# Optimization experiments

Measured on AMD Instinct MI355X. Metric: run time of the kernel, lower is better.

The kernel has to match this reference:

```python
import jax, jax.numpy as jnp
import numpy as np

D_MODEL = 1024
NUM_HEADS = 16
LN_EPS = 1e-5


def setup_inputs() -> dict:
    key = jax.random.key(0)
    ks = jax.random.split(key, 8)
    d = D_MODEL
    x = jax.random.normal(ks[0], (8, 1024, d), dtype=jnp.float32)
    # nn.MultiheadAttention parameters (combined in_proj, out_proj)
    in_proj_w = jax.random.normal(ks[1], (3 * d, d), dtype=jnp.float32) / np.sqrt(d)
    in_proj_b = jnp.zeros((3 * d,), dtype=jnp.float32)
    out_proj_w = jax.random.normal(ks[2], (d, d), dtype=jnp.float32) / np.sqrt(d)
    out_proj_b = jnp.zeros((d,), dtype=jnp.float32)
    ln_w = jnp.ones((d,), dtype=jnp.float32)
    ln_b = jnp.zeros((d,), dtype=jnp.float32)
    time_decay = jnp.asarray(0.1, dtype=jnp.float32)
    return {"x": x, "time_decay": time_decay, "in_proj_w": in_proj_w,
            "in_proj_b": in_proj_b, "out_proj_w": out_proj_w,
            "out_proj_b": out_proj_b, "ln_w": ln_w, "ln_b": ln_b}


def reference(x, time_decay, in_proj_w, in_proj_b, out_proj_w, out_proj_b, ln_w, ln_b):
    B, S, d = x.shape
    H = NUM_HEADS
    hd = d // H
    # vectorized time-decay bias: -|time_decay| * |i - j|  (replaces nested loop)
    idx = jnp.arange(S, dtype=jnp.float32)
    attn_bias = -jnp.abs(time_decay) * jnp.abs(idx[:, None] - idx[None, :])  # [S,S]
    # combined QKV projection
    qkv = x @ in_proj_w.T + in_proj_b  # [B,S,3d]
    q, k, v = jnp.split(qkv, 3, axis=-1)
    q = q.reshape(B, S, H, hd)
    k = k.reshape(B, S, H, hd)
    v = v.reshape(B, S, H, hd)
    scale = 1.0 / np.sqrt(hd)
    scores = jnp.einsum('bqhd,bkhd->bhqk', q, k) * scale + attn_bias  # [B,H,S,S]
    weights = jax.nn.softmax(scores, axis=-1)
    attn = jnp.einsum('bhqk,bkhd->bqhd', weights, v).reshape(B, S, d)
    attn_out = attn @ out_proj_w.T + out_proj_b
    # need_weights=True with default average_attn_weights=True -> mean over heads
    attn_weights = jnp.mean(weights, axis=1)  # [B,S,S]
    # residual + LayerNorm
    y = x + attn_out
    mu = jnp.mean(y, axis=-1, keepdims=True)
    var = jnp.mean(jnp.square(y - mu), axis=-1, keepdims=True)
    out = (y - mu) / jnp.sqrt(var + LN_EPS) * ln_w + ln_b
    return (out, attn_weights)
```

## Files before the change

### kernel.cpp

```cpp
#include <hip/hip_runtime.h>
#include <cstddef>

#define BATCH   8
#define SEQ     1024
#define DMODEL  1024
#define NHEAD   16
#define HDIM    64
#define D3      3072
#define NROWS   (BATCH * SEQ)
#define LN_EPS  1e-5f

typedef __attribute__((ext_vector_type(4))) float f32x4;
typedef __attribute__((ext_vector_type(8))) short bf16x8;

__device__ __forceinline__ float b2f(unsigned short u) {
    union { unsigned int i; float f; } v; v.i = ((unsigned int)u) << 16; return v.f;
}
__device__ __forceinline__ unsigned short f2bu(float f) {
    union { float f; unsigned int i; } v; v.f = f;
    unsigned int r = v.i + 0x7fffu + ((v.i >> 16) & 1u);
    return (unsigned short)(r >> 16);
}
__device__ __forceinline__ void gl16(const void* g, void* l) {
    __builtin_amdgcn_global_load_lds(
        (const __attribute__((address_space(1))) unsigned int*)g,
        (__attribute__((address_space(3))) unsigned int*)l, 16, 0, 0);
}

#define NG_X  1048576
#define NG_WQ 393216
#define NG_WO 131072
__global__ __launch_bounds__(256)
void cvt_bf16(const float* __restrict__ x, const float* __restrict__ wq,
              const float* __restrict__ wo,
              unsigned short* __restrict__ xb, unsigned short* __restrict__ wqb,
              unsigned short* __restrict__ wob) {
    const int gidx = blockIdx.x * 256 + threadIdx.x;
    const float* src; unsigned short* dst; size_t off;
    if (gidx < NG_X)              { src = x;  dst = xb;  off = (size_t)gidx * 8; }
    else if (gidx < NG_X + NG_WQ) { src = wq; dst = wqb; off = (size_t)(gidx - NG_X) * 8; }
    else                          { src = wo; dst = wob; off = (size_t)(gidx - NG_X - NG_WQ) * 8; }
    float4 v0 = *(const float4*)(src + off);
    float4 v1 = *(const float4*)(src + off + 4);
    uint4 pv;
    pv.x = f2bu(v0.x) | ((unsigned int)f2bu(v0.y) << 16);
    pv.y = f2bu(v0.z) | ((unsigned int)f2bu(v0.w) << 16);
    pv.z = f2bu(v1.x) | ((unsigned int)f2bu(v1.y) << 16);
    pv.w = f2bu(v1.z) | ((unsigned int)f2bu(v1.w) << 16);
    *(uint4*)(dst + off) = pv;
}

__global__ __launch_bounds__(256)
void qkv_mfma(const unsigned short* __restrict__ xb,
              const unsigned short* __restrict__ wb,
              const float* __restrict__ bias,
              unsigned short* __restrict__ qh,
              unsigned short* __restrict__ kh,
              unsigned short* __restrict__ vt) {
    __shared__ unsigned short smem[8192];
    unsigned short* As = smem;
    unsigned short* Bs = smem + 4096;

    const int t = threadIdx.x;
    const int w = t >> 6, lane = t & 63;
    const int wm = w >> 1, wn = w & 1;
    const int g = lane >> 4, c = lane & 15;
    const int m0 = blockIdx.y * 128, n0 = blockIdx.x * 128;

    const int srow = t >> 2;
    const int scol = (t & 3) * 8;
    const unsigned short* ga = xb + (size_t)(m0 + srow) * 1024 + scol;
    const unsigned short* gb = wb + (size_t)(n0 + srow) * 1024 + scol;

    f32x4 acc[4][4];
#pragma unroll
    for (int i = 0; i < 4; ++i)
#pragma unroll
        for (int j = 0; j < 4; ++j) acc[i][j] = (f32x4){0.f, 0.f, 0.f, 0.f};

    for (int k0 = 0; k0 < 1024; k0 += 32) {
        gl16(ga + k0,             As + t * 8);
        gl16(ga + 64 * 1024 + k0, As + 2048 + t * 8);
        gl16(gb + k0,             Bs + t * 8);
        gl16(gb + 64 * 1024 + k0, Bs + 2048 + t * 8);
        __syncthreads();
        bf16x8 af[4], bf[4];
#pragma unroll
        for (int i = 0; i < 4; ++i)
            af[i] = *(const bf16x8*)(As + (wm * 64 + i * 16 + c) * 32 + g * 8);
#pragma unroll
        for (int j = 0; j < 4; ++j)
            bf[j] = *(const bf16x8*)(Bs + (wn * 64 + j * 16 + c) * 32 + g * 8);
#pragma unroll
        for (int i = 0; i < 4; ++i)
#pragma unroll
            for (int j = 0; j < 4; ++j)
                acc[i][j] = __builtin_amdgcn_mfma_f32_16x16x32_bf16(af[i], bf[j], acc[i][j], 0, 0, 0);
        __syncthreads();
    }

    float bsv[4];
#pragma unroll
    for (int j = 0; j < 4; ++j) bsv[j] = bias[n0 + wn * 64 + j * 16 + c];

    unsigned short* eslice = smem + w * 2048;
    const int b_ = m0 >> 10;

    if (n0 < 2048) {
        const int ncl   = n0 + wn * 64;
        unsigned short* dst = (ncl < 1024)
            ? qh + ((size_t)(b_ * 16 + (ncl >> 6)) * 1024) * 64
            : kh + ((size_t)(b_ * 16 + ((ncl - 1024) >> 6)) * 1024) * 64;
#pragma unroll
        for (int half = 0; half < 2; ++half) {
#pragma unroll
            for (int ii = 0; ii < 2; ++ii) {
                const int i = half * 2 + ii;
#pragma unroll
                for (int j = 0; j < 4; ++j)
#pragma unroll
                    for (int r = 0; r < 4; ++r)
                        eslice[(ii * 16 + g * 4 + r) * 64 + j * 16 + c] = f2bu(acc[i][j][r] + bsv[j]);
            }
#pragma unroll
            for (int u = 0; u < 4; ++u) {
                const int mloc = u * 8 + (lane >> 3);
                const int ncol = (lane & 7) * 8;
                bf16x8 row = *(const bf16x8*)(eslice + mloc * 64 + ncol);
                const int tok = (m0 & 1023) + wm * 64 + half * 32 + mloc;
                *(bf16x8*)(dst + (size_t)tok * 64 + ncol) = row;
            }
        }
    } else {
        const int key0  = (m0 & 1023) + wm * 64;
        const int hbase = (n0 + wn * 64 - 2048) >> 6;
#pragma unroll
        for (int half = 0; half < 2; ++half) {
#pragma unroll
            for (int jj = 0; jj < 2; ++jj) {
                const int j = half * 2 + jj;
                const int nloc = jj * 16 + c;
#pragma unroll
                for (int i = 0; i < 4; ++i)
#pragma unroll
                    for (int r = 0; r < 4; ++r) {
                        const int mloc  = i * 16 + g * 4 + r;
                        const int mphys = mloc ^ ((nloc & 7) << 3);
                        eslice[nloc * 64 + mphys] = f2bu(acc[i][j][r] + bsv[j]);
                    }
            }
#pragma unroll
            for (int u = 0; u < 4; ++u) {
                const int nloc  = u * 8 + (lane >> 3);
                const int mb    = lane & 7;
                const int mphys = (mb ^ (nloc & 7)) * 8;
                bf16x8 row = *(const bf16x8*)(eslice + nloc * 64 + mphys);
                const int d = half * 32 + nloc;
                *(bf16x8*)(vt + ((size_t)((b_ * 16 + hbase) * 64 + d)) * 1024 + key0 + mb * 8) = row;
            }
        }
    }
}

__global__ __launch_bounds__(512, 2)
void attn_mfma(const unsigned short* __restrict__ qh,
               const unsigned short* __restrict__ kh,
               const unsigned short* __restrict__ vt,
               const float* __restrict__ tdp,
               unsigned short* __restrict__ attnb,
               float* __restrict__ wout) {
    const int flat = blockIdx.x;
    const int b    = flat & 7;
    const int rest = flat >> 3;
    const int hg   = rest >> 4;
    const int qt   = rest & 15;

    const int t  = threadIdx.x;
    const int w  = t >> 6;
    const int lane = t & 63;
    const int g  = lane >> 4;
    const int c  = lane & 15;

    const int q0 = qt * 64;
    const float td2 = -fabsf(tdp[0]) * 1.44269504f;
    const float sc2 = 0.125f * 1.44269504f;

    __shared__ unsigned short P_s[64][1032];
    __shared__ float rs_s[8][64];
    __shared__ float rs_tot[64];
    __shared__ float Ored[4][4][16][17];

    float wsum[4][8][4];
#pragma unroll
    for (int i = 0; i < 4; ++i)
#pragma unroll
        for (int tt = 0; tt < 8; ++tt)
#pragma unroll
            for (int r = 0; r < 4; ++r) wsum[i][tt][r] = 0.f;

    const int key_base = w * 128;
    const float kf0 = (float)(key_base + c);

    for (int hi = 0; hi < 8; ++hi) {
        const int h = hg * 8 + hi;
        const unsigned short* qslab = qh + (size_t)(b * 16 + h) * 1024 * 64;
        const unsigned short* kslab = kh + (size_t)(b * 16 + h) * 1024 * 64;

        bf16x8 qa[4][2];
#pragma unroll
        for (int i = 0; i < 4; ++i) {
            const unsigned short* qp = qslab + (size_t)(q0 + i * 16 + c) * 64 + g * 8;
            qa[i][0] = *(const bf16x8*)(qp);
            qa[i][1] = *(const bf16x8*)(qp + 32);
        }

        float rsum[4][4];
#pragma unroll
        for (int i = 0; i < 4; ++i)
#pragma unroll
            for (int r = 0; r < 4; ++r) rsum[i][r] = 0.f;

#pragma unroll 2
        for (int tt = 0; tt < 8; ++tt) {
            const int key = key_base + tt * 16 + c;
            const unsigned short* kp = kslab + (size_t)key * 64 + g * 8;
            bf16x8 kb0 = *(const bf16x8*)(kp);
            bf16x8 kb1 = *(const bf16x8*)(kp + 32);
            f32x4 z[4];
#pragma unroll
            for (int i = 0; i < 4; ++i) z[i] = (f32x4){0.f, 0.f, 0.f, 0.f};
#pragma unroll
            for (int i = 0; i < 4; ++i)
                z[i] = __builtin_amdgcn_mfma_f32_16x16x32_bf16(qa[i][0], kb0, z[i], 0, 0, 0);
#pragma unroll
            for (int i = 0; i < 4; ++i)
                z[i] = __builtin_amdgcn_mfma_f32_16x16x32_bf16(qa[i][1], kb1, z[i], 0, 0, 0);
            const float kf = kf0 + (float)(tt * 16);
#pragma unroll
            for (int i = 0; i < 4; ++i) {
#pragma unroll
                for (int r = 0; r < 4; ++r) {
                    const float qf = (float)(q0 + i * 16 + g * 4 + r);
                    const float e = __builtin_amdgcn_exp2f(z[i][r] * sc2 + td2 * fabsf(kf - qf));
                    rsum[i][r] += e;
                    P_s[i * 16 + g * 4 + r][key_base + tt * 16 + c] = f2bu(e);
                }
            }
        }
#pragma unroll
        for (int i = 0; i < 4; ++i)
#pragma unroll
            for (int r = 0; r < 4; ++r) {
                rsum[i][r] += __shfl_xor(rsum[i][r], 1, 64);
                rsum[i][r] += __shfl_xor(rsum[i][r], 2, 64);
                rsum[i][r] += __shfl_xor(rsum[i][r], 4, 64);
                rsum[i][r] += __shfl_xor(rsum[i][r], 8, 64);
            }
        if (c == 0) {
#pragma unroll
            for (int i = 0; i < 4; ++i)
#pragma unroll
                for (int r = 0; r < 4; ++r) rs_s[w][i * 16 + g * 4 + r] = rsum[i][r];
        }
        __syncthreads();

        if (t < 64) {
            float s = 0.f;
#pragma unroll
            for (int j = 0; j < 8; ++j) s += rs_s[j][t];
            rs_tot[t] = 1.0f / s;
        }
        __syncthreads();

        float invl[4][4];
#pragma unroll
        for (int i = 0; i < 4; ++i)
#pragma unroll
            for (int r = 0; r < 4; ++r)
                invl[i][r] = rs_tot[i * 16 + g * 4 + r];

        const int dsl = (w & 3) * 16;
        const int ks0 = (w >> 2) * 16;
        f32x4 accO[4];
#pragma unroll
        for (int i = 0; i < 4; ++i) accO[i] = (f32x4){0.f, 0.f, 0.f, 0.f};
        const unsigned short* vhp = vt + (size_t)((b * 16 + h) * 64 + dsl + c) * 1024;
#pragma unroll 4
        for (int ks = ks0; ks < ks0 + 16; ++ks) {
            bf16x8 vb = *(const bf16x8*)(vhp + ks * 32 + g * 8);
#pragma unroll
            for (int i = 0; i < 4; ++i) {
                bf16x8 pa = *(const bf16x8*)(&P_s[i * 16 + c][ks * 32 + g * 8]);
                accO[i] = __builtin_amdgcn_mfma_f32_16x16x32_bf16(pa, vb, accO[i], 0, 0, 0);
            }
        }
        if (w >= 4) {
#pragma unroll
            for (int i = 0; i < 4; ++i)
#pragma unroll
                for (int r = 0; r < 4; ++r)
                    Ored[w - 4][i][g * 4 + r][c] = accO[i][r];
        }
        __syncthreads();
        if (w < 4) {
            unsigned short* op = attnb + (size_t)(b * 1024 + q0) * 1024 + h * 64 + dsl + c;
#pragma unroll
            for (int i = 0; i < 4; ++i)
#pragma unroll
                for (int r = 0; r < 4; ++r) {
                    const float o = accO[i][r] + Ored[w][i][g * 4 + r][c];
                    op[(size_t)(i * 16 + g * 4 + r) * 1024] = f2bu(o * invl[i][r]);
                }
        }

#pragma unroll
        for (int i = 0; i < 4; ++i)
#pragma unroll
            for (int tt = 0; tt < 8; ++tt)
#pragma unroll
                for (int r = 0; r < 4; ++r)
                    wsum[i][tt][r] += b2f(P_s[i * 16 + g * 4 + r][key_base + tt * 16 + c]) * invl[i][r];
        __syncthreads();
    }

#pragma unroll
    for (int i = 0; i < 4; ++i)
#pragma unroll
        for (int tt = 0; tt < 8; ++tt)
#pragma unroll
            for (int r = 0; r < 4; ++r) {
                atomicAdd(&wout[(size_t)(b * 1024 + q0 + i * 16 + g * 4 + r) * 1024
                                 + key_base + tt * 16 + c],
                          wsum[i][tt][r] * (1.0f / NHEAD));
            }
}

__global__ __launch_bounds__(256)
void outproj_mfma(const unsigned short* __restrict__ ab,
                  const unsigned short* __restrict__ wob,
                  const float* __restrict__ bias,
                  const float* __restrict__ X,
                  float* __restrict__ Y) {
    __shared__ unsigned short smem[8192];
    unsigned short* As = smem;
    unsigned short* Bs = smem + 4096;

    const int t = threadIdx.x;
    const int w = t >> 6, lane = t & 63;
    const int wm = w >> 1, wn = w & 1;
    const int g = lane >> 4, c = lane & 15;
    const int m0 = blockIdx.y * 128, n0 = blockIdx.x * 128;

    const int srow = t >> 2;
    const int scol = (t & 3) * 8;
    const unsigned short* ga = ab  + (size_t)(m0 + srow) * 1024 + scol;
    const unsigned short* gb = wob + (size_t)(n0 + srow) * 1024 + scol;

    f32x4 acc[4][4];
#pragma unroll
    for (int i = 0; i < 4; ++i)
#pragma unroll
        for (int j = 0; j < 4; ++j) acc[i][j] = (f32x4){0.f, 0.f, 0.f, 0.f};

    for (int k0 = 0; k0 < 1024; k0 += 32) {
        gl16(ga + k0,             As + t * 8);
        gl16(ga + 64 * 1024 + k0, As + 2048 + t * 8);
        gl16(gb + k0,             Bs + t * 8);
        gl16(gb + 64 * 1024 + k0, Bs + 2048 + t * 8);
        __syncthreads();
        bf16x8 af[4], bf[4];
#pragma unroll
    for (int i = 0; i < 4; ++i)
            af[i] = *(const bf16x8*)(As + (wm * 64 + i * 16 + c) * 32 + g * 8);
#pragma unroll
        for (int j = 0; j < 4; ++j)
            bf[j] = *(const bf16x8*)(Bs + (wn * 64 + j * 16 + c) * 32 + g * 8);
#pragma unroll
        for (int i = 0; i < 4; ++i)
#pragma unroll
            for (int j = 0; j < 4; ++j)
                acc[i][j] = __builtin_amdgcn_mfma_f32_16x16x32_bf16(af[i], bf[j], acc[i][j], 0, 0, 0);
        __syncthreads();
    }

    float bsv[4];
#pragma unroll
    for (int j = 0; j < 4; ++j) bsv[j] = bias[n0 + wn * 64 + j * 16 + c];

#pragma unroll
    for (int i = 0; i < 4; ++i) {
#pragma unroll
        for (int r = 0; r < 4; ++r) {
            const int m = m0 + wm * 64 + i * 16 + g * 4 + r;
#pragma unroll
            for (int j = 0; j < 4; ++j) {
                const int n = n0 + wn * 64 + j * 16 + c;
                Y[(size_t)m * 1024 + n] = acc[i][j][r] + bsv[j] + X[(size_t)m * 1024 + n];
            }
        }
    }
}

__global__ __launch_bounds__(256)
void ln_kernel(const float* __restrict__ Y, const float* __restrict__ lnw,
               const float* __restrict__ lnb, float* __restrict__ out) {
    const int row = blockIdx.x, t = threadIdx.x;
    __shared__ float rs[256], rq[256];
    const float4 v = ((const float4*)(Y + (size_t)row * DMODEL))[t];
    rs[t] = v.x + v.y + v.z + v.w;
    rq[t] = v.x * v.x + v.y * v.y + v.z * v.z + v.w * v.w;
    __syncthreads();
    for (int off = 128; off > 0; off >>= 1) {
        if (t < off) { rs[t] += rs[t + off]; rq[t] += rq[t + off]; }
        __syncthreads();
    }
    const float mu   = rs[0] * (1.0f / DMODEL);
    const float var  = rq[0] * (1.0f / DMODEL) - mu * mu;
    const float rstd = rsqrtf(var + LN_EPS);
    const float4 w  = ((const float4*)lnw)[t];
    const float4 bb = ((const float4*)lnb)[t];
    float4 o;
    o.x = (v.x - mu) * rstd * w.x + bb.x;
    o.y = (v.y - mu) * rstd * w.y + bb.y;
    o.z = (v.z - mu) * rstd * w.z + bb.z;
    o.w = (v.w - mu) * rstd * w.w + bb.w;
    ((float4*)(out + (size_t)row * DMODEL))[t] = o;
}

extern "C" void kernel_launch(void* const* d_in, const int* in_sizes, int n_in,
                              void* d_out, int out_size, void* d_ws, size_t ws_size,
                              hipStream_t stream) {
    (void)in_sizes; (void)n_in; (void)out_size; (void)ws_size;
    const float* x    = (const float*)d_in[0];
    const float* td   = (const float*)d_in[1];
    const float* wqkv = (const float*)d_in[2];
    const float* bqkv = (const float*)d_in[3];
    const float* wo   = (const float*)d_in[4];
    const float* bo   = (const float*)d_in[5];
    const float* lnw  = (const float*)d_in[6];
    const float* lnb  = (const float*)d_in[7];

    float* out_ln = (float*)d_out;
    float* out_w  = (float*)d_out + (size_t)NROWS * SEQ;

    unsigned short* qh = (unsigned short*)d_ws;
    unsigned short* kh = qh + (size_t)128 * 1024 * 64;
    unsigned short* vt = kh + (size_t)128 * 1024 * 64;
    float*          y  = (float*)d_ws;

    unsigned short* attnb = (unsigned short*)d_out;
    unsigned short* wob   = (unsigned short*)d_out + (size_t)NROWS * DMODEL;
    unsigned short* xb    = (unsigned short*)out_w;
    unsigned short* wqkvb = xb + (size_t)NROWS * DMODEL;

    cvt_bf16    <<<(NG_X + NG_WQ + NG_WO) / 256, 256, 0, stream>>>(x, wqkv, wo, xb, wqkvb, wob);
    qkv_mfma    <<<dim3(D3 / 128, NROWS / 128), 256, 0, stream>>>(xb, wqkvb, bqkv, qh, kh, vt);
    (void)hipMemsetAsync(out_w, 0, (size_t)BATCH * SEQ * SEQ * sizeof(float), stream);
    attn_mfma   <<<dim3(256), 512, 0, stream>>>(qh, kh, vt, td, attnb, out_w);
    outproj_mfma<<<dim3(DMODEL / 128, NROWS / 128), 256, 0, stream>>>(attnb, wob, bo, x, y);
    ln_kernel   <<<NROWS,                       256, 0, stream>>>(y, lnw, lnb, out_ln);
}
```

Measured before the change: 420.9 us.

## Split PV work by query tiles and vectorize head-averaged weight accumulation

The P·V stage now assigns each wave two full query-row tiles over all 32 key steps instead of splitting keys across wave halves. This removes the Ored shared-memory cross-wave reduction and one block barrier per head. The head-averaged weight accumulation is remapped so each thread owns a row and 128 contiguous keys, reading P with 16-byte vector loads in a rotated chunk order to spread LDS bank use. Atomics become row-contiguous per thread. In exchange, the per-thread accumulator shape changes and each wave runs a longer serial MFMA chain.

```diff
diff --git a/kernel.cpp b/kernel.cpp
--- a/kernel.cpp
+++ b/kernel.cpp
@@ -188,15 +188,15 @@
     __shared__ unsigned short P_s[64][1032];
     __shared__ float rs_s[8][64];
     __shared__ float rs_tot[64];
-    __shared__ float Ored[4][4][16][17];
-
-    float wsum[4][8][4];
-#pragma unroll
-    for (int i = 0; i < 4; ++i)
-#pragma unroll
-        for (int tt = 0; tt < 8; ++tt)
-#pragma unroll
-            for (int r = 0; r < 4; ++r) wsum[i][tt][r] = 0.f;
+
+    const int wrow = t >> 3;
+    const int wk0  = (t & 7) * 128;
+    const int crot = t & 7;
+    float wsum[16][8];
+#pragma unroll
+    for (int ch = 0; ch < 16; ++ch)
+#pragma unroll
+        for (int e = 0; e < 8; ++e) wsum[ch][e] = 0.f;
 
     const int key_base = w * 128;
     const float kf0 = (float)(key_base + c);
@@ -272,67 +272,56 @@
         }
         __syncthreads();
 
-        float invl[4][4];
-#pragma unroll
-        for (int i = 0; i < 4; ++i)
-#pragma unroll
-            for (int r = 0; r < 4; ++r)
-                invl[i][r] = rs_tot[i * 16 + g * 4 + r];
-
+        const int tb  = (w >> 2) * 2;
         const int dsl = (w & 3) * 16;
-        const int ks0 = (w >> 2) * 16;
-        f32x4 accO[4];
-#pragma unroll
-        for (int i = 0; i < 4; ++i) accO[i] = (f32x4){0.f, 0.f, 0.f, 0.f};
+        f32x4 accO[2];
+        accO[0] = (f32x4){0.f, 0.f, 0.f, 0.f};
+        accO[1] = (f32x4){0.f, 0.f, 0.f, 0.f};
         const unsigned short* vhp = vt + (size_t)((b * 16 + h) * 64 + dsl + c) * 1024;
 #pragma unroll 4
-        for (int ks = ks0; ks < ks0 + 16; ++ks) {
+        for (int ks = 0; ks < 32; ++ks) {
             bf16x8 vb = *(const bf16x8*)(vhp + ks * 32 + g * 8);
 #pragma unroll
-            for (int i = 0; i < 4; ++i) {
-                bf16x8 pa = *(const bf16x8*)(&P_s[i * 16 + c][ks * 32 + g * 8]);
+            for (int i = 0; i < 2; ++i) {
+                bf16x8 pa = *(const bf16x8*)(&P_s[(tb + i) * 16 + c][ks * 32 + g * 8]);
                 accO[i] = __builtin_amdgcn_mfma_f32_16x16x32_bf16(pa, vb, accO[i], 0, 0, 0);
             }
         }
-        if (w >= 4) {
-#pragma unroll
-            for (int i = 0; i < 4; ++i)
-#pragma unroll
-                for (int r = 0; r < 4; ++r)
-                    Ored[w - 4][i][g * 4 + r][c] = accO[i][r];
-        }
-        __syncthreads();
-        if (w < 4) {
+        {
             unsigned short* op = attnb + (size_t)(b * 1024 + q0) * 1024 + h * 64 + dsl + c;
 #pragma unroll
-            for (int i = 0; i < 4; ++i)
+            for (int i = 0; i < 2; ++i)
 #pragma unroll
                 for (int r = 0; r < 4; ++r) {
-                    const float o = accO[i][r] + Ored[w][i][g * 4 + r][c];
-                    op[(size_t)(i * 16 + g * 4 + r) * 1024] = f2bu(o * invl[i][r]);
+                    const int row = (tb + i) * 16 + g * 4 + r;
+                    op[(size_t)row * 1024] = f2bu(accO[i][r] * rs_tot[row]);
                 }
         }
 
-#pragma unroll
-        for (int i = 0; i < 4; ++i)
-#pragma unroll
-            for (int tt = 0; tt < 8; ++tt)
-#pragma unroll
-                for (int r = 0; r < 4; ++r)
-                    wsum[i][tt][r] += b2f(P_s[i * 16 + g * 4 + r][key_base + tt * 16 + c]) * invl[i][r];
-        __syncthreads();
-    }
-
-#pragma unroll
-    for (int i = 0; i < 4; ++i)
-#pragma unroll
-        for (int tt = 0; tt < 8; ++tt)
-#pragma unroll
-            for (int r = 0; r < 4; ++r) {
-                atomicAdd(&wout[(size_t)(b * 1024 + q0 + i * 16 + g * 4 + r) * 1024
-                                 + key_base + tt * 16 + c],
-                          wsum[i][tt][r] * (1.0f / NHEAD));
-            }
+        {
+            const float invr = rs_tot[wrow];
+#pragma unroll
+            for (int cc = 0; cc < 16; ++cc) {
+                const int ch = (cc + crot) & 15;
+                bf16x8 pv = *(const bf16x8*)(&P_s[wrow][wk0 + ch * 8]);
+#pragma unroll
+                for (int e = 0; e < 8; ++e)
+                    wsum[cc][e] += b2f((unsigned short)pv[e]) * invr;
+            }
+        }
+        __syncthreads();
+    }
+
+    {
+        float* wp = wout + (size_t)(b * 1024 + q0 + wrow) * 1024 + wk0;
+#pragma unroll
+        for (int cc = 0; cc < 16; ++cc) {
+            const int ch = (cc + crot) & 15;
+#pragma unroll
+            for (int e = 0; e < 8; ++e)
+                atomicAdd(&wp[ch * 8 + e], wsum[cc][e] * (1.0f / NHEAD));
+        }
+    }
 }
 
 __global__ __launch_bounds__(256)
```

Measured after the change: 1.195 ms. 184% more time.
